# Kernel tuning notes

Measured on AMD Instinct MI355X. Metric: run time of the kernel, lower is better.

Reference implementation:

```python
import jax, jax.numpy as jnp
import numpy as np

B, N, D_IN, D_OUT, R = 8, 1024, 256, 256, 4


def setup_inputs() -> dict:
    key = jax.random.key(0)
    ks = jax.random.split(key, 8)
    scale_in = 1.0 / np.sqrt(D_IN)
    scale_out = 1.0 / np.sqrt(2 * D_OUT)
    scale_g = 1.0 / np.sqrt(D_OUT)
    return {
        "node_features": jax.random.normal(ks[0], (B, N, D_IN), dtype=jnp.float32),
        "adj_matrix": jax.random.randint(ks[1], (B, R, N, N), 0, 2, dtype=jnp.int32),
        "rel_w": jax.random.uniform(ks[2], (R, D_OUT, D_IN), jnp.float32, -scale_in, scale_in),
        "rel_b": jax.random.uniform(ks[3], (R, D_OUT), jnp.float32, -scale_in, scale_in),
        "attn_w": jax.random.uniform(ks[4], (2 * D_OUT,), jnp.float32, -scale_out, scale_out),
        "attn_b": jax.random.uniform(ks[5], (), jnp.float32, -scale_out, scale_out),
        "gate_w": jax.random.uniform(ks[6], (D_OUT,), jnp.float32, -scale_g, scale_g),
        "gate_b": jax.random.uniform(ks[7], (), jnp.float32, -scale_g, scale_g),
    }


def reference(node_features, adj_matrix, rel_w, rel_b, attn_w, attn_b, gate_w, gate_b):
    # Per-relation projections: [B, R, N, D]
    feats = jnp.einsum('bni,rdi->brnd', node_features, rel_w) + rel_b[None, :, None, :]
    # attn_proj(cat([h_i, h_j])) == h_i @ w_i + h_j @ w_j + b  (linear over concat)
    d = feats.shape[-1]
    si = jnp.einsum('brnd,d->brn', feats, attn_w[:d])   # contribution of row node i
    sj = jnp.einsum('brnd,d->brn', feats, attn_w[d:])   # contribution of col node j
    score = si[:, :, :, None] + sj[:, :, None, :] + attn_b  # [B, R, N, N]
    score = jnp.where(adj_matrix == 0, jnp.float32(-1e9), score)
    attn = jax.nn.softmax(score, axis=-1)
    # Aggregate over relations: sum_r attn_r @ feats_r -> [B, N, D]
    agg = jnp.einsum('brnm,brmd->bnd', attn, feats)
    gate = jax.nn.sigmoid(jnp.einsum('bnd,d->bn', agg, gate_w) + gate_b)
    return gate[:, :, None] * agg
```

## Files before the change

### kernel.cpp

```cpp
#include <hip/hip_runtime.h>
#include <hip/hip_bf16.h>

#define B_ 8
#define N_ 1024
#define DIN 256
#define DOUT 256
#define R_ 4

typedef __attribute__((ext_vector_type(8))) short bf16x8;
typedef __attribute__((ext_vector_type(4))) float f32x4;
typedef __attribute__((ext_vector_type(4))) int i32x4;

__device__ __forceinline__ unsigned short f2bf(float f) {
    union { float f; unsigned int u; } v; v.f = f;
    unsigned int u = v.u;
    u += 0x7fffu + ((u >> 16) & 1u);
    return (unsigned short)(u >> 16);
}
__device__ __forceinline__ float bf2f(unsigned short h) {
    union { float f; unsigned int u; } v; v.u = ((unsigned int)h) << 16;
    return v.f;
}

__device__ __forceinline__ void gl_lds16(const void* g, void* l) {
    __builtin_amdgcn_global_load_lds(
        (const __attribute__((address_space(1))) unsigned int*)g,
        (__attribute__((address_space(3))) unsigned int*)l, 16, 0, 0);
}

__global__ __launch_bounds__(256) void k0_swz(const float* __restrict__ rw,
                                              unsigned short* __restrict__ swzW) {
    int t = blockIdx.x * 256 + threadIdx.x;
    int lane = t & 63, nb = (t >> 6) & 15, ks = (t >> 10) & 7, r = t >> 13;
    int m = lane & 15, q = lane >> 4;
    const float* src = rw + ((r * DOUT + nb * 16 + m) * DIN) + ks * 32 + q * 8;
    float4 v0 = *(const float4*)src;
    float4 v1 = *(const float4*)(src + 4);
    bf16x8 o;
    o[0] = (short)f2bf(v0.x); o[1] = (short)f2bf(v0.y);
    o[2] = (short)f2bf(v0.z); o[3] = (short)f2bf(v0.w);
    o[4] = (short)f2bf(v1.x); o[5] = (short)f2bf(v1.y);
    o[6] = (short)f2bf(v1.z); o[7] = (short)f2bf(v1.w);
    *(bf16x8*)(swzW + (long)t * 8) = o;
}

__global__ __launch_bounds__(256) void k1_proj(const float* __restrict__ node,
        const unsigned short* __restrict__ swzW, const float* __restrict__ rel_b,
        const float* __restrict__ attn_w,
        unsigned short* __restrict__ fswz, unsigned short* __restrict__ ebf) {
    __shared__ unsigned short Wbuf[2][8192];
    int bid = blockIdx.x;
    int nt = bid & 15, r = (bid >> 4) & 3, b = bid >> 6;
    int w = threadIdx.x >> 6, lane = threadIdx.x & 63;
    int m = lane & 15, q = lane >> 4;
    int n0 = nt * 64 + w * 16;

    const float* Abase = node + ((b * N_ + n0 + m) * DIN) + q * 8;
    const unsigned short* Wsrc = swzW + r * 65536;

#pragma unroll
    for (int i = 0; i < 4; i++)
        gl_lds16(Wsrc + (w * 4 + i) * 512 + lane * 8, &Wbuf[0][(w * 4 + i) * 512]);

    f32x4 acc[16];
#pragma unroll
    for (int i = 0; i < 16; i++) acc[i] = (f32x4)0.0f;

    float4 a0 = *(const float4*)(Abase);
    float4 a1 = *(const float4*)(Abase + 4);

    for (int ks = 0; ks < 8; ks++) {
        int cur = ks & 1;
        __syncthreads();
        if (ks < 7) {
#pragma unroll
            for (int i = 0; i < 4; i++)
                gl_lds16(Wsrc + ((ks + 1) * 16 + w * 4 + i) * 512 + lane * 8,
                         &Wbuf[cur ^ 1][(w * 4 + i) * 512]);
        }
        bf16x8 af;
        af[0] = (short)f2bf(a0.x); af[1] = (short)f2bf(a0.y);
        af[2] = (short)f2bf(a0.z); af[3] = (short)f2bf(a0.w);
        af[4] = (short)f2bf(a1.x); af[5] = (short)f2bf(a1.y);
        af[6] = (short)f2bf(a1.z); af[7] = (short)f2bf(a1.w);
        if (ks < 7) {
            a0 = *(const float4*)(Abase + (ks + 1) * 32);
            a1 = *(const float4*)(Abase + (ks + 1) * 32 + 4);
        }
#pragma unroll
        for (int nb = 0; nb < 16; nb++) {
            bf16x8 wf = *(const bf16x8*)(&Wbuf[cur][nb * 512 + lane * 8]);
            acc[nb] = __builtin_amdgcn_mfma_f32_16x16x32_bf16(af, wf, acc[nb], 0, 0, 0);
        }
    }

    float sj0 = 0.f, sj1 = 0.f, sj2 = 0.f, sj3 = 0.f;
    float bias[16], aw[16];
#pragma unroll
    for (int nb = 0; nb < 16; nb++) {
        int d = nb * 16 + m;
        bias[nb] = rel_b[r * DOUT + d];
        aw[nb] = attn_w[DOUT + d];
        sj0 += (acc[nb][0] + bias[nb]) * aw[nb];
        sj1 += (acc[nb][1] + bias[nb]) * aw[nb];
        sj2 += (acc[nb][2] + bias[nb]) * aw[nb];
        sj3 += (acc[nb][3] + bias[nb]) * aw[nb];
    }
#pragma unroll
    for (int mk = 1; mk <= 8; mk <<= 1) {
        sj0 += __shfl_xor(sj0, mk, 64);
        sj1 += __shfl_xor(sj1, mk, 64);
        sj2 += __shfl_xor(sj2, mk, 64);
        sj3 += __shfl_xor(sj3, mk, 64);
    }
    float e0 = __expf(sj0), e1 = __expf(sj1), e2 = __expf(sj2), e3 = __expf(sj3);

    int slice = b * R_ + r;
    int js = n0 >> 5;
    int jhi = (n0 >> 4) & 1;
    int qp = jhi * 2 + (q >> 1);
    int jj0 = (q & 1) * 4;
    unsigned short* fb = fswz + ((long)(slice * 32 + js) * 16) * 512
                       + qp * 128 + m * 8 + jj0;
#pragma unroll
    for (int nb = 0; nb < 16; nb++) {
        ushort4 o;
        o.x = f2bf((acc[nb][0] + bias[nb]) * e0);
        o.y = f2bf((acc[nb][1] + bias[nb]) * e1);
        o.z = f2bf((acc[nb][2] + bias[nb]) * e2);
        o.w = f2bf((acc[nb][3] + bias[nb]) * e3);
        *(ushort4*)(fb + nb * 512) = o;
    }
    if (m == 0) {
        ushort4 o;
        o.x = f2bf(e0); o.y = f2bf(e1); o.z = f2bf(e2); o.w = f2bf(e3);
        *(ushort4*)(ebf + slice * N_ + n0 + q * 4) = o;
    }
}

__global__ __launch_bounds__(256, 4) void k3_attn(const int* __restrict__ adj,
        const unsigned short* __restrict__ fswz, const unsigned short* __restrict__ ebf,
        unsigned short* __restrict__ aggU, float* __restrict__ lbuf) {
    __shared__ unsigned short Gbuf[2][8192];
    __shared__ unsigned short Ebuf[512];

    int bid = blockIdx.x;
    int slice = (bid & 7) * 4 + ((bid >> 3) & 3);
    int rest = bid >> 5;
    int it = rest & 15, jh = rest >> 4;
    int t = threadIdx.x, lane = t & 63, w = t >> 6;
    int m = lane & 15, q = lane >> 4;
    int i0b = it * 64;

    const unsigned short* fsl = fswz + ((size_t)(slice * 32 + jh * 16)) * 8192;
    const int* adjbase = adj + (size_t)slice * (N_ * N_)
                       + (size_t)(i0b + w * 16 + m) * N_ + jh * 512 + q * 8;
    const unsigned short* esl = ebf + slice * N_ + jh * 512;

#pragma unroll
    for (int i = 0; i < 4; i++)
        gl_lds16(fsl + (w * 4 + i) * 512 + lane * 8, &Gbuf[0][(w * 4 + i) * 512]);
    if (w == 0)
        gl_lds16(esl + lane * 8, &Ebuf[0]);

    i32x4 A0c = *(const i32x4*)(adjbase);
    i32x4 A1c = *(const i32x4*)(adjbase + 4);

    f32x4 acc[16];
#pragma unroll
    for (int i = 0; i < 16; i++) acc[i] = (f32x4)0.0f;
    float l = 0.f;

    for (int s = 0; s < 16; s++) {
        int cur = s & 1;
        __syncthreads();
        i32x4 A0n, A1n;
        if (s < 15) {
#pragma unroll
            for (int i = 0; i < 4; i++)
                gl_lds16(fsl + (size_t)(s + 1) * 8192 + (w * 4 + i) * 512 + lane * 8,
                         &Gbuf[cur ^ 1][(w * 4 + i) * 512]);
            A0n = *(const i32x4*)(adjbase + (s + 1) * 32);
            A1n = *(const i32x4*)(adjbase + (s + 1) * 32 + 4);
        }
        bf16x8 ev = *(const bf16x8*)(&Ebuf[s * 32 + q * 8]);
        int av[8] = {A0c.x, A0c.y, A0c.z, A0c.w, A1c.x, A1c.y, A1c.z, A1c.w};
        const int* ei = (const int*)&ev;
        bf16x8 af;
        int* afi = (int*)&af;
#pragma unroll
        for (int p = 0; p < 4; p++) {
            unsigned int msk = (av[2 * p] ? 0xffffu : 0u)
                             | (av[2 * p + 1] ? 0xffff0000u : 0u);
            afi[p] = (int)(msk & 0x3F803F80u);
            int me = ei[p] & (int)msk;
            union { int i; float f; } lo, hi;
            lo.i = me << 16;
            hi.i = me & (int)0xffff0000u;
            l += lo.f + hi.f;
        }
        const unsigned short* Gb = &Gbuf[cur][lane * 8];
#pragma unroll
        for (int nb = 0; nb < 16; nb++) {
            bf16x8 bfq = *(const bf16x8*)(Gb + nb * 512);
            acc[nb] = __builtin_amdgcn_mfma_f32_16x16x32_bf16(af, bfq, acc[nb], 0, 0, 0);
        }
        A0c = A0n; A1c = A1n;
    }

    l += __shfl_xor(l, 16, 64);
    l += __shfl_xor(l, 32, 64);
    int half = slice * 2 + jh;
    if (lane < 16)
        lbuf[half * N_ + i0b + w * 16 + lane] = l;

    unsigned short* ob = aggU + ((size_t)half * N_ + i0b + w * 16 + q * 4) * DOUT + m;
#pragma unroll
    for (int nb = 0; nb < 16; nb++) {
#pragma unroll
        for (int reg = 0; reg < 4; reg++)
            ob[(size_t)reg * DOUT + nb * 16] = f2bf(acc[nb][reg]);
    }
}

__global__ __launch_bounds__(256) void k4_out(const unsigned short* __restrict__ aggU,
        const float* __restrict__ lbuf, const float* __restrict__ gate_w,
        const float* __restrict__ gate_b, float* __restrict__ out) {
    __shared__ float red[4];
    int bid = blockIdx.x;
    int n = bid & 1023, b = bid >> 10;
    int d = threadIdx.x;
    float s = 0.f;
#pragma unroll
    for (int r = 0; r < R_; r++) {
        int sl = b * R_ + r;
        float a0 = bf2f(aggU[((size_t)(sl * 2 + 0) * N_ + n) * DOUT + d]);
        float a1 = bf2f(aggU[((size_t)(sl * 2 + 1) * N_ + n) * DOUT + d]);
        float lt = lbuf[(sl * 2 + 0) * N_ + n] + lbuf[(sl * 2 + 1) * N_ + n];
        float inv = (lt > 0.f) ? 1.0f / lt : 0.f;
        s += (a0 + a1) * inv;
    }
    float v = s * gate_w[d];
#pragma unroll
    for (int off = 32; off; off >>= 1) v += __shfl_down(v, off, 64);
    int lane = d & 63, wave = d >> 6;
    if (lane == 0) red[wave] = v;
    __syncthreads();
    float tot = red[0] + red[1] + red[2] + red[3];
    float g = 1.f / (1.f + __expf(-(tot + gate_b[0])));
    out[((long)(b * N_ + n)) * DOUT + d] = g * s;
}

extern "C" void kernel_launch(void* const* d_in, const int* in_sizes, int n_in,
                              void* d_out, int out_size, void* d_ws, size_t ws_size,
                              hipStream_t stream) {
    const float* node   = (const float*)d_in[0];
    const int*   adj    = (const int*)d_in[1];
    const float* rel_w  = (const float*)d_in[2];
    const float* rel_b  = (const float*)d_in[3];
    const float* attn_w = (const float*)d_in[4];
    const float* gate_w = (const float*)d_in[6];
    const float* gate_b = (const float*)d_in[7];
    float* out = (float*)d_out;

    char* ws = (char*)d_ws;
    unsigned short* swzW = (unsigned short*)ws;
    unsigned short* fswz = (unsigned short*)(ws + 524288);
    unsigned short* ebf  = (unsigned short*)(ws + 17301504);
    unsigned short* aggU = (unsigned short*)(ws + 17367040);
    float*          lbuf = (float*)(ws + 50921472);

    k0_swz<<<128, 256, 0, stream>>>(rel_w, swzW);
    k1_proj<<<512, 256, 0, stream>>>(node, swzW, rel_b, attn_w, fswz, ebf);
    k3_attn<<<1024, 256, 0, stream>>>(adj, fswz, ebf, aggU, lbuf);
    k4_out<<<8192, 256, 0, stream>>>(aggU, lbuf, gate_w, gate_b, out);
}
```

Baseline: 252.6 us.

## Add producer warp with triple-buffered LDS and flag-based sync in attention kernel

Adds a fifth wavefront to the attention kernel. It alone streams feature tiles into a triple-buffered LDS ring. Consumer waves spin on shared-memory flags and signal buffer release with atomic counters, replacing the block-wide barrier each step. The goal is to overlap global-to-LDS loads with MFMA work and remove barrier stalls, at the cost of more LDS per block (which may lower occupancy), spin-wait overhead, and reliance on LDS visibility ordering for correctness.

```diff
diff --git a/kernel.cpp b/kernel.cpp
--- a/kernel.cpp
+++ b/kernel.cpp
@@ -27,6 +27,9 @@
         (const __attribute__((address_space(1))) unsigned int*)g,
         (__attribute__((address_space(3))) unsigned int*)l, 16, 0, 0);
 }
+
+#define WAIT_VM0   0x3F70
+#define WAIT_LGKM0 0xC07F
 
 __global__ __launch_bounds__(256) void k0_swz(const float* __restrict__ rw,
                                               unsigned short* __restrict__ swzW) {
@@ -138,11 +141,13 @@
     }
 }
 
-__global__ __launch_bounds__(256, 4) void k3_attn(const int* __restrict__ adj,
+__global__ __launch_bounds__(320, 4) void k3_attn(const int* __restrict__ adj,
         const unsigned short* __restrict__ fswz, const unsigned short* __restrict__ ebf,
         unsigned short* __restrict__ aggU, float* __restrict__ lbuf) {
-    __shared__ unsigned short Gbuf[2][8192];
+    __shared__ unsigned short Gbuf[3][8192];
     __shared__ unsigned short Ebuf[512];
+    __shared__ int vflag[3];
+    __shared__ int vcons[3];
 
     int bid = blockIdx.x;
     int slice = (bid & 7) * 4 + ((bid >> 3) & 3);
@@ -153,15 +158,40 @@
     int i0b = it * 64;
 
     const unsigned short* fsl = fswz + ((size_t)(slice * 32 + jh * 16)) * 8192;
+    const unsigned short* esl = ebf + slice * N_ + jh * 512;
+
+    if (t < 3) { vflag[t] = 0; vcons[t] = 0; }
+    __syncthreads();
+
+    if (w == 4) {
+        gl_lds16(esl + lane * 8, &Ebuf[0]);
+#pragma unroll 1
+        for (int s = 0; s < 3; s++) {
+            const unsigned short* src = fsl + (size_t)s * 8192;
+#pragma unroll
+            for (int i = 0; i < 16; i++)
+                gl_lds16(src + i * 512 + lane * 8, &Gbuf[s][i * 512]);
+            __builtin_amdgcn_s_waitcnt(WAIT_VM0);
+            if (lane == 0) ((volatile int*)vflag)[s] = s + 1;
+        }
+#pragma unroll 1
+        for (int s = 3; s < 16; s++) {
+            int b3 = s % 3;
+            while (((volatile int*)vcons)[b3] < 4) { }
+            __builtin_amdgcn_s_waitcnt(WAIT_LGKM0);
+            if (lane == 0) ((volatile int*)vcons)[b3] = 0;
+            const unsigned short* src = fsl + (size_t)s * 8192;
+#pragma unroll
+            for (int i = 0; i < 16; i++)
+                gl_lds16(src + i * 512 + lane * 8, &Gbuf[b3][i * 512]);
+            __builtin_amdgcn_s_waitcnt(WAIT_VM0);
+            if (lane == 0) ((volatile int*)vflag)[b3] = s + 1;
+        }
+        return;
+    }
+
     const int* adjbase = adj + (size_t)slice * (N_ * N_)
                        + (size_t)(i0b + w * 16 + m) * N_ + jh * 512 + q * 8;
-    const unsigned short* esl = ebf + slice * N_ + jh * 512;
-
-#pragma unroll
-    for (int i = 0; i < 4; i++)
-        gl_lds16(fsl + (w * 4 + i) * 512 + lane * 8, &Gbuf[0][(w * 4 + i) * 512]);
-    if (w == 0)
-        gl_lds16(esl + lane * 8, &Ebuf[0]);
 
     i32x4 A0c = *(const i32x4*)(adjbase);
     i32x4 A1c = *(const i32x4*)(adjbase + 4);
@@ -171,18 +201,16 @@
     for (int i = 0; i < 16; i++) acc[i] = (f32x4)0.0f;
     float l = 0.f;
 
+#pragma unroll 1
     for (int s = 0; s < 16; s++) {
-        int cur = s & 1;
-        __syncthreads();
+        int b3 = s % 3;
         i32x4 A0n, A1n;
         if (s < 15) {
-#pragma unroll
-            for (int i = 0; i < 4; i++)
-                gl_lds16(fsl + (size_t)(s + 1) * 8192 + (w * 4 + i) * 512 + lane * 8,
-                         &Gbuf[cur ^ 1][(w * 4 + i) * 512]);
             A0n = *(const i32x4*)(adjbase + (s + 1) * 32);
             A1n = *(const i32x4*)(adjbase + (s + 1) * 32 + 4);
         }
+        while (((volatile int*)vflag)[b3] < s + 1) { }
+
         bf16x8 ev = *(const bf16x8*)(&Ebuf[s * 32 + q * 8]);
         int av[8] = {A0c.x, A0c.y, A0c.z, A0c.w, A1c.x, A1c.y, A1c.z, A1c.w};
         const int* ei = (const int*)&ev;
@@ -199,12 +227,14 @@
             hi.i = me & (int)0xffff0000u;
             l += lo.f + hi.f;
         }
-        const unsigned short* Gb = &Gbuf[cur][lane * 8];
+        const unsigned short* Gb = &Gbuf[b3][lane * 8];
 #pragma unroll
         for (int nb = 0; nb < 16; nb++) {
             bf16x8 bfq = *(const bf16x8*)(Gb + nb * 512);
             acc[nb] = __builtin_amdgcn_mfma_f32_16x16x32_bf16(af, bfq, acc[nb], 0, 0, 0);
         }
+        __builtin_amdgcn_s_waitcnt(WAIT_LGKM0);
+        if (lane == 0) atomicAdd(&vcons[b3], 1);
         A0c = A0n; A1c = A1n;
     }
 
@@ -272,6 +302,6 @@
 
     k0_swz<<<128, 256, 0, stream>>>(rel_w, swzW);
     k1_proj<<<512, 256, 0, stream>>>(node, swzW, rel_b, attn_w, fswz, ebf);
-    k3_attn<<<1024, 256, 0, stream>>>(adj, fswz, ebf, aggU, lbuf);
+    k3_attn<<<1024, 320, 0, stream>>>(adj, fswz, ebf, aggU, lbuf);
     k4_out<<<8192, 256, 0, stream>>>(aggU, lbuf, gate_w, gate_b, out);
 }
```

New measurement: 269.2 us. +6.6%, slower.

## Pre-pack adjacency into bitmasks in a separate kernel before attention

Applied to the files above, without the earlier changes.

Adds a k2_pack kernel that reads the int32 adjacency matrix and uses wave ballots to compress each row into 64-bit bitmasks. The attention kernel then loads one row's whole 16-word mask up front, extracting per-step bytes instead of streaming int32 adjacency inside its MFMA loop. The aim is to take the large adjacency read off k3's critical path and shrink k3's global traffic. The cost is an extra kernel launch and a separate full pass over the adjacency tensor, so total DRAM traffic is roughly unchanged.

```diff
diff --git a/kernel.cpp b/kernel.cpp
--- a/kernel.cpp
+++ b/kernel.cpp
@@ -138,7 +138,25 @@
     }
 }
 
-__global__ __launch_bounds__(256, 4) void k3_attn(const int* __restrict__ adj,
+__global__ __launch_bounds__(256) void k2_pack(const int* __restrict__ adj,
+                                               unsigned long long* __restrict__ pk) {
+    int w = threadIdx.x >> 6, lane = threadIdx.x & 63;
+    long rowbase = (long)blockIdx.x * 32 + w * 8;
+#pragma unroll 1
+    for (int rr = 0; rr < 8; rr++) {
+        long row = rowbase + rr;
+        const int* src = adj + row * N_ + lane;
+        unsigned long long* dst = pk + row * 16;
+#pragma unroll
+        for (int kk = 0; kk < 16; kk++) {
+            int a = src[kk * 64];
+            unsigned long long bm = __ballot(a != 0);
+            if (lane == 0) dst[kk] = bm;
+        }
+    }
+}
+
+__global__ __launch_bounds__(256, 4) void k3_attn(const unsigned int* __restrict__ pk,
         const unsigned short* __restrict__ fswz, const unsigned short* __restrict__ ebf,
         unsigned short* __restrict__ aggU, float* __restrict__ lbuf) {
     __shared__ unsigned short Gbuf[2][8192];
@@ -153,9 +171,15 @@
     int i0b = it * 64;
 
     const unsigned short* fsl = fswz + ((size_t)(slice * 32 + jh * 16)) * 8192;
-    const int* adjbase = adj + (size_t)slice * (N_ * N_)
-                       + (size_t)(i0b + w * 16 + m) * N_ + jh * 512 + q * 8;
     const unsigned short* esl = ebf + slice * N_ + jh * 512;
+
+    const unsigned int* pb = pk + ((size_t)slice * N_ + i0b + w * 16 + m) * 32 + jh * 16;
+    unsigned int Wv[16];
+    *(i32x4*)(&Wv[0])  = *(const i32x4*)(pb);
+    *(i32x4*)(&Wv[4])  = *(const i32x4*)(pb + 4);
+    *(i32x4*)(&Wv[8])  = *(const i32x4*)(pb + 8);
+    *(i32x4*)(&Wv[12]) = *(const i32x4*)(pb + 12);
+    int q8 = q * 8;
 
 #pragma unroll
     for (int i = 0; i < 4; i++)
@@ -163,35 +187,30 @@
     if (w == 0)
         gl_lds16(esl + lane * 8, &Ebuf[0]);
 
-    i32x4 A0c = *(const i32x4*)(adjbase);
-    i32x4 A1c = *(const i32x4*)(adjbase + 4);
-
     f32x4 acc[16];
 #pragma unroll
     for (int i = 0; i < 16; i++) acc[i] = (f32x4)0.0f;
     float l = 0.f;
 
+#pragma unroll
     for (int s = 0; s < 16; s++) {
         int cur = s & 1;
         __syncthreads();
-        i32x4 A0n, A1n;
         if (s < 15) {
 #pragma unroll
             for (int i = 0; i < 4; i++)
                 gl_lds16(fsl + (size_t)(s + 1) * 8192 + (w * 4 + i) * 512 + lane * 8,
                          &Gbuf[cur ^ 1][(w * 4 + i) * 512]);
-            A0n = *(const i32x4*)(adjbase + (s + 1) * 32);
-            A1n = *(const i32x4*)(adjbase + (s + 1) * 32 + 4);
-        }
+        }
+        unsigned int byte = (Wv[s] >> q8) & 0xffu;
         bf16x8 ev = *(const bf16x8*)(&Ebuf[s * 32 + q * 8]);
-        int av[8] = {A0c.x, A0c.y, A0c.z, A0c.w, A1c.x, A1c.y, A1c.z, A1c.w};
         const int* ei = (const int*)&ev;
         bf16x8 af;
         int* afi = (int*)&af;
 #pragma unroll
         for (int p = 0; p < 4; p++) {
-            unsigned int msk = (av[2 * p] ? 0xffffu : 0u)
-                             | (av[2 * p + 1] ? 0xffff0000u : 0u);
+            unsigned int msk = (((byte >> (2 * p)) & 1u) ? 0xffffu : 0u)
+                             | (((byte >> (2 * p + 1)) & 1u) ? 0xffff0000u : 0u);
             afi[p] = (int)(msk & 0x3F803F80u);
             int me = ei[p] & (int)msk;
             union { int i; float f; } lo, hi;
@@ -205,7 +224,6 @@
             bf16x8 bfq = *(const bf16x8*)(Gb + nb * 512);
             acc[nb] = __builtin_amdgcn_mfma_f32_16x16x32_bf16(af, bfq, acc[nb], 0, 0, 0);
         }
-        A0c = A0n; A1c = A1n;
     }
 
     l += __shfl_xor(l, 16, 64);
@@ -269,9 +287,11 @@
     unsigned short* ebf  = (unsigned short*)(ws + 17301504);
     unsigned short* aggU = (unsigned short*)(ws + 17367040);
     float*          lbuf = (float*)(ws + 50921472);
+    unsigned long long* pk = (unsigned long long*)(ws + 51183616);
 
     k0_swz<<<128, 256, 0, stream>>>(rel_w, swzW);
+    k2_pack<<<1024, 256, 0, stream>>>(adj, pk);
     k1_proj<<<512, 256, 0, stream>>>(node, swzW, rel_b, attn_w, fswz, ebf);
-    k3_attn<<<1024, 256, 0, stream>>>(adj, fswz, ebf, aggU, lbuf);
+    k3_attn<<<1024, 256, 0, stream>>>((const unsigned int*)pk, fswz, ebf, aggU, lbuf);
     k4_out<<<8192, 256, 0, stream>>>(aggU, lbuf, gate_w, gate_b, out);
 }
```

Result: slower. 320.6 us (+26.9%).
